# Optimization experiments

Measured on AMD Instinct MI355X. Metric: run time of the kernel, lower is better.

Reference implementation:

```python
import jax, jax.numpy as jnp
import numpy as np

B, L, D, K_F = 2, 1024, 768, 16  # batch, seq_len, n_embd, num_eigh**2
N_FFT = 2048


def setup_inputs() -> dict:
    key = jax.random.key(0)
    k1, k2, k3, k4 = jax.random.split(key, 4)
    x = jax.random.normal(k1, (B, L, D), dtype=jnp.float32)
    phi = jax.random.normal(k2, (L, K_F), dtype=jnp.float32) * 0.1
    M_phi_plus = jax.random.normal(k3, (K_F, D, D), dtype=jnp.float32) * (1.0 / np.sqrt(K_F * D))
    M_phi_minus = jax.random.normal(k4, (K_F, D, D), dtype=jnp.float32) * (1.0 / np.sqrt(K_F * D))
    return {"x": x, "phi": phi, "M_phi_plus": M_phi_plus, "M_phi_minus": M_phi_minus, "n": N_FFT}


def _convolve(u, v, n):
    """FFT causal convolution with K spectral filters (flash-stu `convolve`, use_approx=False).
    u: [B, L, D] inputs; v: [L, K] filters; n: FFT length (>= 2L-1 padded pow2).
    Returns U_plus, U_minus: [B, L, K, D].
    """
    b, l, d = u.shape
    sgn = jnp.where(jnp.arange(l) % 2 == 0, 1.0, -1.0).astype(u.dtype)  # alternating +/-
    # Stack the plain and sign-modulated signals: [B, L, 1, D, 2]
    U = jnp.stack([u, u * sgn[None, :, None]], axis=-1)[:, :, None, :, :]
    Uf = jnp.fft.rfft(U, n=n, axis=1)                      # [B, F, 1, D, 2] complex
    vf = jnp.fft.rfft(v, n=n, axis=0)[None, :, :, None, None]  # [1, F, K, 1, 1]
    conv = jnp.fft.irfft(vf * Uf, n=n, axis=1)[:, :l]      # [B, L, K, D, 2]
    U_plus = conv[..., 0]
    U_minus = conv[..., 1] * sgn[None, :, None, None]
    return U_plus, U_minus


def reference(x, phi, M_phi_plus, M_phi_minus, n):
    U_plus, U_minus = _convolve(x, phi, n)
    # tensordot(U, M, dims=([2,3],[0,2])): contract eigenmode k and input channel i
    spectral_plus = jnp.einsum('blki,koi->blo', U_plus, M_phi_plus)
    spectral_minus = jnp.einsum('blki,koi->blo', U_minus, M_phi_minus)
    return spectral_plus + spectral_minus
```

## Files before the change

kernel.cpp:

```cpp
#include <hip/hip_runtime.h>
#include <hip/hip_fp16.h>

typedef unsigned short u16;
typedef unsigned int   u32;
typedef _Float16 f16;
typedef __attribute__((ext_vector_type(8))) f16 f16x8;
typedef __attribute__((ext_vector_type(2))) __fp16 fp16x2;
typedef __attribute__((ext_vector_type(4))) float f32x4;

#define B_SZ  2
#define L_SEQ 1024
#define D_EMB 768
#define KF    16
#define MDIM  (B_SZ * L_SEQ)
#define KROW  (KF * D_EMB)
#define MELEM ((size_t)KF * D_EMB * D_EMB)
#define NTILE 96
#define PT_SZ 16384

__device__ __forceinline__ void gload16(const void* g, void* l) {
    __builtin_amdgcn_global_load_lds(
        (const __attribute__((address_space(1))) u32*)g,
        (__attribute__((address_space(3))) u32*)l, 16, 0, 0);
}

__global__ __launch_bounds__(256) void stu_setup(const float* __restrict__ x,
                                                 const float* __restrict__ phi,
                                                 u16* __restrict__ xT,
                                                 u16* __restrict__ Ttab) {
    __shared__ __align__(16) float xs[64][68];
    const int bid = blockIdx.x;
    const int tid = threadIdx.x;

    if (bid < 384) {
        const int s0 = (bid & 15) << 6;
        const int d0 = ((bid >> 4) % 12) << 6;
        const int b  = bid / 192;

#pragma unroll
        for (int j = 0; j < 4; ++j) {
            int c = tid + (j << 8);
            int row = c >> 4;
            int col = (c & 15) << 2;
            *(float4*)&xs[row][col] =
                *(const float4*)&x[((size_t)b * L_SEQ + s0 + row) * D_EMB + d0 + col];
        }
        __syncthreads();

        const int dl = tid >> 2;
        const int ss = (tid & 3) << 4;
        const int dg = d0 + dl;
        const int xorv = (dg & 7) << 3;

        union { u16 v[16]; uint4 q[2]; } pk;
#pragma unroll
        for (int u = 0; u < 16; ++u)
            pk.v[u] = __half_as_ushort(__float2half(xs[ss + u][dl]));

        size_t base = (size_t)b * D_EMB * L_SEQ + (size_t)dg * L_SEQ + s0;
        *(uint4*)&xT[base + ( ss      ^ xorv)] = pk.q[0];
        *(uint4*)&xT[base + ((ss + 8) ^ xorv)] = pk.q[1];
    } else {
        const int f = bid - 384;
        const int q = f & 15;
        const int k = f >> 4;
        const int tt  = tid >> 2;
        const int ss0 = (tid & 3) << 4;

        union { u16 v[16]; uint4 q4[2]; } pk;
#pragma unroll
        for (int u = 0; u < 16; ++u) {
            int s = (q << 6) + tt - (ss0 + u);
            float v = (s >= 0 && s < L_SEQ) ? phi[s * KF + k] : 0.f;
            pk.v[u] = __half_as_ushort(__float2half(v));
        }
        const int xorv = (tt & 7) << 3;
        u16* tile = Ttab + (((size_t)k * 16 + q) << 12);
        *(uint4*)&tile[(tt << 6) + ( ss0      ^ xorv)] = pk.q4[0];
        *(uint4*)&tile[(tt << 6) + ((ss0 + 8) ^ xorv)] = pk.q4[1];
    }
}

__global__ __launch_bounds__(256) void stu_conv_mcvt(
        const u16* __restrict__ xT, const u16* __restrict__ Ttab,
        u16* __restrict__ Up, u16* __restrict__ Um,
        const float* __restrict__ Mp, const float* __restrict__ Mm,
        u16* __restrict__ Hp, u16* __restrict__ Hm) {
    __shared__ __align__(16) u16 Xs[2][192 * 64];
    __shared__ __align__(16) u16 Tps[2][64 * 64];

    const int bid = blockIdx.x;
    const int tid = threadIdx.x;

    if (bid < 512) {
        const size_t n8 = MELEM / 8;
        size_t i = (size_t)bid * 256 + tid;
        const size_t stride = (size_t)512 * 256;
        for (size_t cc = i; cc < n8; cc += stride) {
            const size_t g = cc << 3;
            {
                const float4 a0 = *(const float4*)&Mp[g];
                const float4 a1 = *(const float4*)&Mp[g + 4];
                union { fp16x2 h2[4]; uint4 q; } u;
                u.h2[0] = __builtin_amdgcn_cvt_pkrtz(a0.x, a0.y);
                u.h2[1] = __builtin_amdgcn_cvt_pkrtz(a0.z, a0.w);
                u.h2[2] = __builtin_amdgcn_cvt_pkrtz(a1.x, a1.y);
                u.h2[3] = __builtin_amdgcn_cvt_pkrtz(a1.z, a1.w);
                *(uint4*)&Hp[g] = u.q;
            }
            {
                const float4 a0 = *(const float4*)&Mm[g];
                const float4 a1 = *(const float4*)&Mm[g + 4];
                union { fp16x2 h2[4]; uint4 q; } u;
                u.h2[0] = __builtin_amdgcn_cvt_pkrtz(a0.x, a0.y);
                u.h2[1] = __builtin_amdgcn_cvt_pkrtz(a0.z, a0.w);
                u.h2[2] = __builtin_amdgcn_cvt_pkrtz(a1.x, a1.y);
                u.h2[3] = __builtin_amdgcn_cvt_pkrtz(a1.z, a1.w);
                *(uint4*)&Hm[g] = u.q;
            }
        }
        return;
    }

    const int c    = bid - 512;
    const int xcd  = c & 7;
    const int w    = c >> 3;
    const int ti   = 15 - (w >> 4);
    const int t0   = ti << 6;
    const int inner = w & 15;
    const int bk   = (xcd << 2) + (inner >> 2);
    const int b    = bk >> 4;
    const int k    = bk & 15;
    const int d0   = (inner & 3) * 192;

    const int lane = tid & 63;
    const int wid  = tid >> 6;
    const int wr   = wid >> 1;
    const int wc   = wid & 1;
    const int lr   = lane & 15;
    const int lk   = lane >> 4;

    const u32 xm = (lr & 1) ? 0x00008000u : 0x80000000u;

    f32x4 acc[2][2][6];
#pragma unroll
    for (int s = 0; s < 2; ++s)
#pragma unroll
        for (int m = 0; m < 2; ++m)
#pragma unroll
            for (int n = 0; n < 6; ++n)
                acc[s][m][n] = (f32x4){0.f, 0.f, 0.f, 0.f};

    const u16* xTb = xT + (size_t)b * D_EMB * L_SEQ + (size_t)d0 * L_SEQ;
    const u16* Tpk = Ttab + ((size_t)k << 16);

    auto stageX = [&](int buf, int r0) {
#pragma unroll
        for (int j = 0; j < 6; ++j) {
            int cc = tid + (j << 8);
            gload16(xTb + (size_t)(cc >> 3) * L_SEQ + r0 + ((cc & 7) << 3),
                    &Xs[buf][cc << 3]);
        }
    };
    auto stageT = [&](int buf, int q) {
        const u16* tp = Tpk + ((size_t)q << 12);
        gload16(tp + (tid << 3),         &Tps[buf][tid << 3]);
        gload16(tp + ((tid + 256) << 3), &Tps[buf][(tid + 256) << 3]);
    };

    stageX(0, 0);
    stageT(0, ti);
    __syncthreads();

    int cur = 0;
    for (int r0 = 0; r0 <= t0; r0 += 64) {
        if (r0 < t0) {
            stageT(cur ^ 1, ((t0 - r0) >> 6) - 1);
            stageX(cur ^ 1, r0 + 64);
        }

        const char* XsC = (const char*)&Xs[cur][0];
        const char* TpC = (const char*)&Tps[cur][0];

#pragma unroll
        for (int kk = 0; kk < 2; ++kk) {
            f16x8 bfr[6];
#pragma unroll
            for (int n = 0; n < 6; ++n) {
                const int row = wc * 96 + (n << 4) + lr;
                const int boff = ((kk << 6) + (lk << 4)) ^ ((row & 7) << 4);
                bfr[n] = *(const f16x8*)(XsC + row * 128 + boff);
            }
#pragma unroll
            for (int m = 0; m < 2; ++m) {
                const int rowt = (wr << 5) + (m << 4) + lr;
                const int aoff = ((kk << 6) + (lk << 4)) ^ ((rowt & 7) << 4);
                const f16x8 ap = *(const f16x8*)(TpC + rowt * 128 + aoff);
                union { f16x8 h; u32 wv[4]; } cv;
                cv.h = ap;
#pragma unroll
                for (int qd = 0; qd < 4; ++qd) cv.wv[qd] ^= xm;
                const f16x8 am = cv.h;
#pragma unroll
                for (int n = 0; n < 6; ++n) {
                    acc[0][m][n] = __builtin_amdgcn_mfma_f32_16x16x32_f16(
                        ap, bfr[n], acc[0][m][n], 0, 0, 0);
                    acc[1][m][n] = __builtin_amdgcn_mfma_f32_16x16x32_f16(
                        am, bfr[n], acc[1][m][n], 0, 0, 0);
                }
            }
        }
        __syncthreads();
        cur ^= 1;
    }

#pragma unroll
    for (int m = 0; m < 2; ++m) {
        const int trow = t0 + (wr << 5) + (m << 4) + (lk << 2);
#pragma unroll
        for (int n = 0; n < 6; ++n) {
            const int col = d0 + wc * 96 + (n << 4) + lr;
#pragma unroll
            for (int j = 0; j < 4; ++j) {
                size_t idx = ((size_t)(b * L_SEQ + trow + j) * KF + k) * D_EMB + col;
                Up[idx] = __half_as_ushort(__float2half(acc[0][m][n][j]));
                Um[idx] = __half_as_ushort(__float2half(acc[1][m][n][j]));
            }
        }
    }
}

__global__ __launch_bounds__(256) void stu_spectral_mfma(
        const u16* __restrict__ Up, const u16* __restrict__ Um,
        const u16* __restrict__ Mhp, const u16* __restrict__ Mhm,
        float* __restrict__ out, u16* __restrict__ P, int usePartial) {
    __shared__ __align__(16) u16 As[128 * 64];
    __shared__ __align__(16) u16 Bs[128 * 64];

    const int h   = blockIdx.x;
    const int z   = h & 7;
    const int rem = h >> 3;
    const int o0  = (rem % 6) << 7;
    const int m0  = (rem / 6) << 7;
    const int sign = z & 1;
    const int k0 = (z >> 1) << 2;

    const u16* A    = sign ? Um : Up;
    const u16* Bsrc = sign ? Mhm : Mhp;

    const int tid  = threadIdx.x;
    const int lane = tid & 63;
    const int wid  = tid >> 6;
    const int wr   = wid >> 1;
    const int wc   = wid & 1;
    const int lr   = lane & 15;
    const int lk   = lane >> 4;

    f32x4 acc[4][4];
#pragma unroll
    for (int m = 0; m < 4; ++m)
#pragma unroll
        for (int n = 0; n < 4; ++n)
            acc[m][n] = (f32x4){0.f, 0.f, 0.f, 0.f};

    for (int k = k0; k < k0 + 4; ++k) {
        const u16* Ak = A + (size_t)m0 * KROW + k * D_EMB;
        const u16* Bk = Bsrc + (size_t)k * D_EMB * D_EMB + (size_t)o0 * D_EMB;

        for (int ic = 0; ic < D_EMB; ic += 64) {
            __syncthreads();
#pragma unroll
            for (int j = 0; j < 4; ++j) {
                const int c = tid + (j << 8);
                const int row = c >> 3;
                const int off = ((c & 7) ^ (row & 7)) << 3;
                gload16(Ak + (size_t)row * KROW + ic + off, &As[c << 3]);
                gload16(Bk + (size_t)row * D_EMB + ic + off, &Bs[c << 3]);
            }
            __syncthreads();

#pragma unroll
            for (int kk = 0; kk < 2; ++kk) {
                f16x8 af[4], bf[4];
#pragma unroll
                for (int m = 0; m < 4; ++m) {
                    const int row = wr * 64 + (m << 4) + lr;
                    const int boff = (((kk << 2) + lk) ^ (row & 7)) << 4;
                    af[m] = *(const f16x8*)((const char*)&As[0] + row * 128 + boff);
                }
#pragma unroll
                for (int n = 0; n < 4; ++n) {
                    const int row = wc * 64 + (n << 4) + lr;
                    const int boff = (((kk << 2) + lk) ^ (row & 7)) << 4;
                    bf[n] = *(const f16x8*)((const char*)&Bs[0] + row * 128 + boff);
                }
#pragma unroll
                for (int m = 0; m < 4; ++m)
#pragma unroll
                    for (int n = 0; n < 4; ++n)
                        acc[m][n] = __builtin_amdgcn_mfma_f32_16x16x32_f16(
                            af[m], bf[n], acc[m][n], 0, 0, 0);
            }
        }
    }

    if (usePartial) {
        u16* Pt = P + (size_t)h * PT_SZ;
#pragma unroll
        for (int m = 0; m < 4; ++m) {
            const int rowl = wr * 64 + (m << 4) + (lk << 2);
#pragma unroll
            for (int n = 0; n < 4; ++n) {
                const int coll = wc * 64 + (n << 4) + lr;
#pragma unroll
                for (int j = 0; j < 4; ++j)
                    Pt[(rowl + j) * 128 + coll] =
                        __half_as_ushort(__float2half(acc[m][n][j]));
            }
        }
    } else {
#pragma unroll
        for (int m = 0; m < 4; ++m) {
            const int row = m0 + wr * 64 + (m << 4) + (lk << 2);
#pragma unroll
            for (int n = 0; n < 4; ++n) {
                const int col = o0 + wc * 64 + (n << 4) + lr;
#pragma unroll
                for (int j = 0; j < 4; ++j)
                    atomicAdd(&out[(size_t)(row + j) * D_EMB + col], acc[m][n][j]);
            }
        }
    }
}

__global__ __launch_bounds__(256) void stu_reduce(const u16* __restrict__ P,
                                                  float* __restrict__ out) {
    const int g    = blockIdx.x * 256 + threadIdx.x;
    const int row  = g / 96;
    const int col0 = (g % 96) << 3;
    const int tile = (row >> 7) * 6 + (col0 >> 7);
    const u16* p = P + (size_t)tile * 8 * PT_SZ + ((row & 127) << 7) + (col0 & 127);

    float s[8] = {0.f, 0.f, 0.f, 0.f, 0.f, 0.f, 0.f, 0.f};
#pragma unroll
    for (int z = 0; z < 8; ++z) {
        const uint4 q = *(const uint4*)(p + (size_t)z * PT_SZ);
        union { uint4 q; u16 v[8]; } u;
        u.q = q;
#pragma unroll
        for (int j = 0; j < 8; ++j)
            s[j] += __half2float(__ushort_as_half(u.v[j]));
    }
    const size_t ob = (size_t)row * D_EMB + col0;
    *(float4*)&out[ob]     = (float4){s[0], s[1], s[2], s[3]};
    *(float4*)&out[ob + 4] = (float4){s[4], s[5], s[6], s[7]};
}

extern "C" void kernel_launch(void* const* d_in, const int* in_sizes, int n_in,
                              void* d_out, int out_size, void* d_ws, size_t ws_size,
                              hipStream_t stream) {
    const float* x   = (const float*)d_in[0];
    const float* phi = (const float*)d_in[1];
    const float* Mp  = (const float*)d_in[2];
    const float* Mm  = (const float*)d_in[3];
    float* out = (float*)d_out;

    const size_t S = (size_t)MDIM * KROW;
    u16* Up   = (u16*)d_ws;
    u16* Um   = Up + S;
    u16* Mhp  = Um + S;
    u16* Mhm  = Mhp + MELEM;
    u16* xT   = Mhm + MELEM;
    u16* Ttab = xT + (size_t)B_SZ * D_EMB * L_SEQ;
    u16* Part = Ttab + (size_t)KF * 16 * 4096;

    const size_t elems_needed = 2 * S + 2 * MELEM + 1572864 + 1048576 + 12582912;
    const int usePartial = (ws_size >= elems_needed * sizeof(u16)) ? 1 : 0;

    if (!usePartial)
        (void)hipMemsetAsync(d_out, 0, (size_t)out_size * sizeof(float), stream);

    stu_setup<<<dim3(640), dim3(256), 0, stream>>>(x, phi, xT, Ttab);

    stu_conv_mcvt<<<dim3(2560), dim3(256), 0, stream>>>(
        xT, Ttab, Up, Um, Mp, Mm, Mhp, Mhm);

    stu_spectral_mfma<<<dim3(NTILE * 8), dim3(256), 0, stream>>>(
        Up, Um, Mhp, Mhm, out, Part, usePartial);

    if (usePartial)
        stu_reduce<<<dim3(768), dim3(256), 0, stream>>>(Part, out);
}
```

Baseline: 168.0 us.

## Double-buffer spectral GEMM LDS tiles and use partial vmcnt waits

The spectral GEMM kernel now keeps two LDS buffers for A and B and flattens the k/ic loops into one 48-iteration loop. It prefetches the next tile with global_load_lds while computing on the current one. Both the conv and spectral kernels replace __syncthreads with explicit s_waitcnt vmcnt(8/0) plus raw s_barrier, so only the current tile's loads are waited on. This adds LDS use, which may lower occupancy, and relies on hand-counted vmcnt values being correct.

```diff
diff --git a/kernel.cpp b/kernel.cpp
--- a/kernel.cpp
+++ b/kernel.cpp
@@ -23,6 +23,9 @@
         (const __attribute__((address_space(1))) u32*)g,
         (__attribute__((address_space(3))) u32*)l, 16, 0, 0);
 }
+
+#define VMCNT8() asm volatile("s_waitcnt vmcnt(8)" ::: "memory")
+#define VMCNT0() asm volatile("s_waitcnt vmcnt(0)" ::: "memory")
 
 __global__ __launch_bounds__(256) void stu_setup(const float* __restrict__ x,
                                                  const float* __restrict__ phi,
@@ -170,14 +173,16 @@
 
     stageX(0, 0);
     stageT(0, ti);
-    __syncthreads();
 
     int cur = 0;
     for (int r0 = 0; r0 <= t0; r0 += 64) {
-        if (r0 < t0) {
+        const int more = (r0 < t0);
+        if (more) {
             stageT(cur ^ 1, ((t0 - r0) >> 6) - 1);
             stageX(cur ^ 1, r0 + 64);
         }
+        if (more) { VMCNT8(); } else { VMCNT0(); }
+        __builtin_amdgcn_s_barrier();
 
         const char* XsC = (const char*)&Xs[cur][0];
         const char* TpC = (const char*)&Tps[cur][0];
@@ -210,7 +215,7 @@
                 }
             }
         }
-        __syncthreads();
+        __builtin_amdgcn_s_barrier();
         cur ^= 1;
     }
 
@@ -234,8 +239,8 @@
         const u16* __restrict__ Up, const u16* __restrict__ Um,
         const u16* __restrict__ Mhp, const u16* __restrict__ Mhm,
         float* __restrict__ out, u16* __restrict__ P, int usePartial) {
-    __shared__ __align__(16) u16 As[128 * 64];
-    __shared__ __align__(16) u16 Bs[128 * 64];
+    __shared__ __align__(16) u16 As[2][128 * 64];
+    __shared__ __align__(16) u16 Bs[2][128 * 64];
 
     const int h   = blockIdx.x;
     const int z   = h & 7;
@@ -263,45 +268,55 @@
         for (int n = 0; n < 4; ++n)
             acc[m][n] = (f32x4){0.f, 0.f, 0.f, 0.f};
 
-    for (int k = k0; k < k0 + 4; ++k) {
-        const u16* Ak = A + (size_t)m0 * KROW + k * D_EMB;
-        const u16* Bk = Bsrc + (size_t)k * D_EMB * D_EMB + (size_t)o0 * D_EMB;
-
-        for (int ic = 0; ic < D_EMB; ic += 64) {
-            __syncthreads();
-#pragma unroll
-            for (int j = 0; j < 4; ++j) {
-                const int c = tid + (j << 8);
-                const int row = c >> 3;
-                const int off = ((c & 7) ^ (row & 7)) << 3;
-                gload16(Ak + (size_t)row * KROW + ic + off, &As[c << 3]);
-                gload16(Bk + (size_t)row * D_EMB + ic + off, &Bs[c << 3]);
-            }
-            __syncthreads();
-
-#pragma unroll
-            for (int kk = 0; kk < 2; ++kk) {
-                f16x8 af[4], bf[4];
-#pragma unroll
-                for (int m = 0; m < 4; ++m) {
-                    const int row = wr * 64 + (m << 4) + lr;
-                    const int boff = (((kk << 2) + lk) ^ (row & 7)) << 4;
-                    af[m] = *(const f16x8*)((const char*)&As[0] + row * 128 + boff);
-                }
-#pragma unroll
-                for (int n = 0; n < 4; ++n) {
-                    const int row = wc * 64 + (n << 4) + lr;
-                    const int boff = (((kk << 2) + lk) ^ (row & 7)) << 4;
-                    bf[n] = *(const f16x8*)((const char*)&Bs[0] + row * 128 + boff);
-                }
-#pragma unroll
-                for (int m = 0; m < 4; ++m)
-#pragma unroll
-                    for (int n = 0; n < 4; ++n)
-                        acc[m][n] = __builtin_amdgcn_mfma_f32_16x16x32_f16(
-                            af[m], bf[n], acc[m][n], 0, 0, 0);
-            }
-        }
+    auto stage = [&](int buf, int it) {
+        const int k  = k0 + it / 12;
+        const int ic = (it % 12) << 6;
+        const u16* Ak = A + (size_t)m0 * KROW + (size_t)k * D_EMB + ic;
+        const u16* Bk = Bsrc + ((size_t)k * D_EMB + o0) * D_EMB + ic;
+#pragma unroll
+        for (int j = 0; j < 4; ++j) {
+            const int cch = tid + (j << 8);
+            const int row = cch >> 3;
+            const int off = ((cch & 7) ^ (row & 7)) << 3;
+            gload16(Ak + (size_t)row * KROW + off, &As[buf][cch << 3]);
+            gload16(Bk + (size_t)row * D_EMB + off, &Bs[buf][cch << 3]);
+        }
+    };
+
+    stage(0, 0);
+
+    for (int it = 0; it < 48; ++it) {
+        const int cur = it & 1;
+        const int more = (it < 47);
+        if (more) stage(cur ^ 1, it + 1);
+        if (more) { VMCNT8(); } else { VMCNT0(); }
+        __builtin_amdgcn_s_barrier();
+
+        const char* AsC = (const char*)&As[cur][0];
+        const char* BsC = (const char*)&Bs[cur][0];
+#pragma unroll
+        for (int kk = 0; kk < 2; ++kk) {
+            f16x8 af[4], bf[4];
+#pragma unroll
+            for (int m = 0; m < 4; ++m) {
+                const int row = wr * 64 + (m << 4) + lr;
+                const int boff = (((kk << 2) + lk) ^ (row & 7)) << 4;
+                af[m] = *(const f16x8*)(AsC + row * 128 + boff);
+            }
+#pragma unroll
+            for (int n = 0; n < 4; ++n) {
+                const int row = wc * 64 + (n << 4) + lr;
+                const int boff = (((kk << 2) + lk) ^ (row & 7)) << 4;
+                bf[n] = *(const f16x8*)(BsC + row * 128 + boff);
+            }
+#pragma unroll
+            for (int m = 0; m < 4; ++m)
+#pragma unroll
+                for (int n = 0; n < 4; ++n)
+                    acc[m][n] = __builtin_amdgcn_mfma_f32_16x16x32_f16(
+                        af[m], bf[n], acc[m][n], 0, 0, 0);
+        }
+        __builtin_amdgcn_s_barrier();
     }
 
     if (usePartial) {
```

New measurement: 199.6 us. 18.8% more time.
